# Performance work log

Measured on AMD Instinct MI355X. Metric: run time of the kernel, lower is better.

## Reference

```python
import jax, jax.numpy as jnp
import numpy as np

EMBED_DIM = 1024
NUM_HEADS = 16
HEAD_DIM = EMBED_DIM // NUM_HEADS


def setup_inputs() -> dict:
    key = jax.random.key(0)
    ks = jax.random.split(key, 6)
    std = 0.02
    x = jax.random.normal(ks[0], (2, 2048, EMBED_DIM), dtype=jnp.float32)
    Wq = jax.random.normal(ks[1], (EMBED_DIM, EMBED_DIM), dtype=jnp.float32) * std
    Wk = jax.random.normal(ks[2], (EMBED_DIM, EMBED_DIM), dtype=jnp.float32) * std
    Wv = jax.random.normal(ks[3], (EMBED_DIM, EMBED_DIM), dtype=jnp.float32) * std
    Wo = jax.random.normal(ks[4], (EMBED_DIM, EMBED_DIM), dtype=jnp.float32) * std
    Wf = jax.random.normal(ks[5], (NUM_HEADS, EMBED_DIM), dtype=jnp.float32) * std
    return {"x": x, "Wq": Wq, "Wk": Wk, "Wv": Wv, "Wo": Wo, "Wf": Wf}


def reference(x, Wq, Wk, Wv, Wo, Wf):
    b, n, d = x.shape
    h, hd = NUM_HEADS, HEAD_DIM
    # projections (nn.Linear without bias: y = x @ W^T)
    q = (x @ Wq.T).reshape(b, n, h, hd)
    k = (x @ Wk.T).reshape(b, n, h, hd)
    v = (x @ Wv.T).reshape(b, n, h, hd)
    # per-head log forget gate and its causal cumulative sum
    log_f = jax.nn.log_sigmoid(x @ Wf.T)          # [b, n, h]
    c = jnp.cumsum(log_f, axis=1)                 # [b, n, h], c_i = sum_{t<=i} log f_t
    cbh = c.transpose(0, 2, 1)                    # [b, h, n]
    scale = 1.0 / np.sqrt(hd).astype(np.float32)
    # scores s_ij = q_i.k_j * scale + (c_i - c_j)  (decay D_ij = sum_{t=j+1}^i log f_t)
    scores = jnp.einsum("bihd,bjhd->bhij", q, k) * scale
    scores = scores + cbh[:, :, :, None] - cbh[:, :, None, :]
    causal = jnp.tril(jnp.ones((n, n), dtype=bool))
    scores = jnp.where(causal, scores, -1e30)
    p = jax.nn.softmax(scores, axis=-1)           # [b, h, n, n]
    out = jnp.einsum("bhij,bjhd->bihd", p, v).reshape(b, n, d)
    return out @ Wo.T
```

## Files before the change

### kernel.cpp

```cpp
#include <hip/hip_runtime.h>

#define EMBED 1024
#define NHEAD 16
#define HD    64
#define SEQ   2048
#define BATCH 2
#define ROWS  (BATCH * SEQ)

typedef float f32x4 __attribute__((ext_vector_type(4)));
typedef short short8 __attribute__((ext_vector_type(8)));
typedef short short4v __attribute__((ext_vector_type(4)));
typedef unsigned short u16x4 __attribute__((ext_vector_type(4)));
typedef unsigned short u16x8 __attribute__((ext_vector_type(8)));
typedef unsigned u32x4 __attribute__((ext_vector_type(4)));
typedef unsigned u32x2 __attribute__((ext_vector_type(2)));

#define LOG2E 1.4426950408889634f

__device__ __forceinline__ unsigned short f2bf(float f) {
  unsigned int u = __builtin_bit_cast(unsigned int, f);
  u += 0x7fffu + ((u >> 16) & 1u);
  return (unsigned short)(u >> 16);
}

__device__ __forceinline__ unsigned cvtpk(float lo, float hi) {
  unsigned r;
  asm("v_cvt_pk_bf16_f32 %0, %1, %2" : "=v"(r) : "v"(lo), "v"(hi));
  return r;
}

#if __has_builtin(__builtin_amdgcn_exp2f)
#define EXP2(x) __builtin_amdgcn_exp2f(x)
#else
#define EXP2(x) exp2f(x)
#endif

__device__ __forceinline__ void gll16(const void* g, const void* l) {
  __builtin_amdgcn_global_load_lds(
      (const __attribute__((address_space(1))) unsigned int*)g,
      (__attribute__((address_space(3))) unsigned int*)l, 16, 0, 0);
}

__device__ __forceinline__ unsigned lds_addr(const void* p) {
  return (unsigned)(size_t)(__attribute__((address_space(3))) const void*)p;
}

__global__ __launch_bounds__(256) void cvt_all_kernel(
    const float* __restrict__ x,
    const float* __restrict__ w0, const float* __restrict__ w1,
    const float* __restrict__ w2, const float* __restrict__ w3,
    const float* __restrict__ wf,
    unsigned short* __restrict__ xo,
    unsigned short* __restrict__ o0, unsigned short* __restrict__ o1,
    unsigned short* __restrict__ o2, unsigned short* __restrict__ o3,
    unsigned short* __restrict__ wfh, unsigned short* __restrict__ wfl,
    unsigned* __restrict__ qkmaxu) {
  const int y = blockIdx.y;
  if (y < 4) {
    const float* in = (y == 0) ? w0 : (y == 1) ? w1 : (y == 2) ? w2 : w3;
    unsigned short* out = (y == 0) ? o0 : (y == 1) ? o1 : (y == 2) ? o2 : o3;
    const int i = blockIdx.x * 256 + threadIdx.x;
    const f32x4 v0 = reinterpret_cast<const f32x4*>(in)[2 * i];
    const f32x4 v1 = reinterpret_cast<const f32x4*>(in)[2 * i + 1];
    u16x8 o;
#pragma unroll
    for (int e = 0; e < 4; ++e) { o[e] = f2bf(v0[e]); o[e + 4] = f2bf(v1[e]); }
    reinterpret_cast<u16x8*>(out)[i] = o;
  } else if (y == 4) {
#pragma unroll
    for (int e = 0; e < 4; ++e) {
      const int i = e * 131072 + blockIdx.x * 256 + threadIdx.x;
      const f32x4 v0 = reinterpret_cast<const f32x4*>(x)[2 * i];
      const f32x4 v1 = reinterpret_cast<const f32x4*>(x)[2 * i + 1];
      u16x8 h;
#pragma unroll
      for (int q = 0; q < 4; ++q) { h[q] = f2bf(v0[q]); h[q + 4] = f2bf(v1[q]); }
      reinterpret_cast<u16x8*>(xo)[i] = h;
    }
  } else {
    if (blockIdx.x < 8) {
      const int i = blockIdx.x * 256 + threadIdx.x;
      const f32x4 v0 = reinterpret_cast<const f32x4*>(wf)[2 * i];
      const f32x4 v1 = reinterpret_cast<const f32x4*>(wf)[2 * i + 1];
      u16x8 h, l;
#pragma unroll
      for (int q = 0; q < 4; ++q) {
        h[q] = f2bf(v0[q]);
        l[q] = f2bf(v0[q] - __builtin_bit_cast(float, (unsigned)h[q] << 16));
        h[q + 4] = f2bf(v1[q]);
        l[q + 4] = f2bf(v1[q] - __builtin_bit_cast(float, (unsigned)h[q + 4] << 16));
      }
      reinterpret_cast<u16x8*>(wfh)[i] = h;
      reinterpret_cast<u16x8*>(wfl)[i] = l;
    } else if (blockIdx.x == 8) {
      if (threadIdx.x < 64) qkmaxu[threadIdx.x] = 0u;
    }
  }
}

__global__ __launch_bounds__(256) void gemm_wo_kernel(
    const unsigned short* __restrict__ A, const unsigned short* __restrict__ B,
    float* __restrict__ C) {
  __shared__ unsigned short Asm[64 * 64];
  __shared__ unsigned short Bsm[64 * 64];
  const int tid = threadIdx.x, wid = tid >> 6, lane = tid & 63;
  const int g = lane >> 4, l16 = lane & 15;
  const int wr = wid >> 1, wc = wid & 1;
  const int mb = blockIdx.y;
  const int nb = blockIdx.x;

  f32x4 acc[2][2] = {};

  for (int k0 = 0; k0 < EMBED; k0 += 64) {
    __syncthreads();
#pragma unroll
    for (int q = 0; q < 2; ++q) {
      const int base = (wid * 2 + q) * 1024;
      const int off = base + lane * 16;
      const int row = off >> 7;
      const int colel = (off & 127) >> 1;
      gll16(A + (size_t)(mb * 64 + row) * EMBED + k0 + colel, (const char*)Asm + base);
      gll16(B + (size_t)(nb * 64 + row) * EMBED + k0 + colel, (const char*)Bsm + base);
    }
    __syncthreads();

#pragma unroll
    for (int kc = 0; kc < 2; ++kc) {
      short8 am[2], bm[2];
#pragma unroll
      for (int mi = 0; mi < 2; ++mi)
        am[mi] = *reinterpret_cast<const short8*>(&Asm[(wr * 32 + mi * 16 + l16) * 64 + kc * 32 + g * 8]);
#pragma unroll
      for (int ni = 0; ni < 2; ++ni)
        bm[ni] = *reinterpret_cast<const short8*>(&Bsm[(wc * 32 + ni * 16 + l16) * 64 + kc * 32 + g * 8]);
#pragma unroll
      for (int mi = 0; mi < 2; ++mi)
#pragma unroll
        for (int ni = 0; ni < 2; ++ni)
          acc[mi][ni] = __builtin_amdgcn_mfma_f32_16x16x32_bf16(am[mi], bm[ni], acc[mi][ni], 0, 0, 0);
    }
  }

#pragma unroll
  for (int mi = 0; mi < 2; ++mi)
#pragma unroll
    for (int ni = 0; ni < 2; ++ni)
#pragma unroll
      for (int r = 0; r < 4; ++r) {
        const int m = mb * 64 + wr * 32 + mi * 16 + g * 4 + r;
        const int n = nb * 64 + wc * 32 + ni * 16 + l16;
        C[(size_t)m * EMBED + n] = acc[mi][ni][r];
      }
}

#define BAR() asm volatile("s_barrier" ::: "memory")
#define LGKM0()                                              \
  do {                                                       \
    asm volatile("s_waitcnt lgkmcnt(0)" ::: "memory");       \
    __builtin_amdgcn_sched_barrier(0);                       \
  } while (0)
#define VM(n_) asm volatile("s_waitcnt vmcnt(" #n_ ")" ::: "memory")

__global__ __launch_bounds__(512, 2) void gemm256_kernel(
    const unsigned short* __restrict__ A,
    const unsigned short* __restrict__ B0, const unsigned short* __restrict__ B1,
    const unsigned short* __restrict__ B2,
    unsigned short* __restrict__ C0, unsigned short* __restrict__ C1,
    unsigned short* __restrict__ C2, unsigned* __restrict__ qkmaxu,
    const float* __restrict__ x, const unsigned short* __restrict__ wfh,
    const unsigned short* __restrict__ wfl, float* __restrict__ carr) {
  __shared__ unsigned short sm[2][2][2][8192];
  const int tid = threadIdx.x, wid = tid >> 6, lane = tid & 63;
  const int g = lane >> 4, l16 = lane & 15;

  if (blockIdx.x >= 192) {
    const int bid2 = blockIdx.x - 192;
    const int tile = bid2 * 4 + (wid >> 1);
    const int half = wid & 1;
    const int row0 = tile * 16;
    const int k0 = half * 512;
    const float* xp = x + (size_t)(row0 + l16) * EMBED + k0 + g * 8;
    const unsigned short* whp = wfh + (size_t)l16 * EMBED + k0 + g * 8;
    const unsigned short* wlp = wfl + (size_t)l16 * EMBED + k0 + g * 8;
    f32x4 acc = {};
#pragma unroll
    for (int k = 0; k < 16; ++k) {
      const f32x4 v0 = *reinterpret_cast<const f32x4*>(xp + k * 32);
      const f32x4 v1 = *reinterpret_cast<const f32x4*>(xp + k * 32 + 4);
      short8 ah, al;
#pragma unroll
      for (int e = 0; e < 4; ++e) {
        const unsigned short h0 = f2bf(v0[e]);
        ah[e] = (short)h0;
        al[e] = (short)f2bf(v0[e] - __builtin_bit_cast(float, (unsigned)h0 << 16));
        const unsigned short h1 = f2bf(v1[e]);
        ah[e + 4] = (short)h1;
        al[e + 4] = (short)f2bf(v1[e] - __builtin_bit_cast(float, (unsigned)h1 << 16));
      }
      const short8 bh = *reinterpret_cast<const short8*>(whp + k * 32);
      const short8 bl = *reinterpret_cast<const short8*>(wlp + k * 32);
      acc = __builtin_amdgcn_mfma_f32_16x16x32_bf16(ah, bh, acc, 0, 0, 0);
      acc = __builtin_amdgcn_mfma_f32_16x16x32_bf16(ah, bl, acc, 0, 0, 0);
      acc = __builtin_amdgcn_mfma_f32_16x16x32_bf16(al, bh, acc, 0, 0, 0);
    }
    f32x4* red = reinterpret_cast<f32x4*>(sm);
    red[wid * 64 + lane] = acc;
    __syncthreads();
    if (half == 0) {
      const f32x4 a = red[wid * 64 + lane] + red[(wid + 1) * 64 + lane];
#pragma unroll
      for (int r = 0; r < 4; ++r) {
        const float s = a[r];
        const float ls = (fminf(s, 0.f) - log1pf(__expf(-fabsf(s)))) * LOG2E;
        const int n = row0 + g * 4 + r;
        const int b = n >> 11, nn = n & (SEQ - 1);
        carr[(size_t)(b * NHEAD + l16) * SEQ + nn] = ls;
      }
    }
    return;
  }

  const int wr = wid >> 2, wcol = wid & 3;
  const int mb = blockIdx.x / 12;
  const int nb = blockIdx.x % 12;
  const int which = nb >> 2;
  const int col0 = (nb & 3) * 256;
  const unsigned short* Bp = (which == 0) ? B0 : (which == 1) ? B1 : B2;
  unsigned short* Cp = (which == 0) ? C0 : (which == 1) ? C1 : C2;

  const int lane8 = lane & 7, laneHi = lane >> 3;
  const int colel = (lane8 ^ laneHi) * 8;
  int soff[2];
#pragma unroll
  for (int q = 0; q < 2; ++q)
    soff[q] = (q * 64 + wid * 8 + laneHi) * EMBED + colel;
  const unsigned short* Ag = A + (size_t)(mb * 256) * EMBED;
  const unsigned short* Bg = Bp + (size_t)col0 * EMBED;

  const int sw = (l16 & 7) << 4;
  const int cs0 = (0 | (g * 16)) ^ sw;
  const int cs1 = (64 | (g * 16)) ^ sw;
  const char* smB = (const char*)sm;
  const int aBase = wr * 16384 + l16 * 128;
  const int bBase = 32768 + (wcol >> 1) * 16384 + (wcol & 1) * 8192 + l16 * 128;

#define STG(buf_, ab_, half_, gsrc_, t_)                                               \
  do {                                                                                 \
    const unsigned short* gp_ = (gsrc_) + (size_t)(half_) * (128 * EMBED) + (t_) * 64; \
    char* lp_ = (char*)sm + (buf_) * 65536 + (ab_) * 32768 + (half_) * 16384 + wid * 1024; \
    gll16(gp_ + soff[0], lp_);                                                         \
    gll16(gp_ + soff[1], lp_ + 8192);                                                  \
  } while (0)

#define RD_A(buf_, row_, kc_) \
  (*reinterpret_cast<const short8*>(smB + (buf_) * 65536 + aBase + (row_) * 2048 + ((kc_) ? cs1 : cs0)))
#define RD_B(buf_, row_, kc_) \
  (*reinterpret_cast<const short8*>(smB + (buf_) * 65536 + bBase + (row_) * 2048 + ((kc_) ? cs1 : cs0)))

#define QUAD(mg_, ng_)                                                                   \
  do {                                                                                   \
    __builtin_amdgcn_s_setprio(1);                                                       \
    _Pragma("unroll") for (int kc_ = 0; kc_ < 2; ++kc_)                                  \
      _Pragma("unroll") for (int mi_ = 0; mi_ < 4; ++mi_)                                \
        _Pragma("unroll") for (int nj_ = 0; nj_ < 2; ++nj_)                              \
          acc[(mg_) * 4 + mi_][(ng_) * 2 + nj_] = __builtin_amdgcn_mfma_f32_16x16x32_bf16( \
              fa[mi_][kc_], fb[(ng_) * 2 + nj_][kc_], acc[(mg_) * 4 + mi_][(ng_) * 2 + nj_], 0, 0, 0); \
    __builtin_amdgcn_s_setprio(0);                                                       \
  } while (0)

#define KTILE4(BUF_, STG_P1, STG_P2, STG_P3, STG_P4_VM)                                  \
  do {                                                                                   \
    _Pragma("unroll") for (int mi_ = 0; mi_ < 4; ++mi_) {                                \
      fa[mi_][0] = RD_A(BUF_, mi_, 0);                                                   \
      fa[mi_][1] = RD_A(BUF_, mi_, 1);                                                   \
    }                                                                                    \
    _Pragma("unroll") for (int ni_ = 0; ni_ < 2; ++ni_) {                                \
      fb[ni_][0] = RD_B(BUF_, ni_, 0);                                                   \
      fb[ni_][1] = RD_B(BUF_, ni_, 1);                                                   \
    }                                                                                    \
    STG_P1;                                                                              \
    asm volatile("s_waitcnt lgkmcnt(8)" ::: "memory");                                   \
    BAR();                                                                               \
    LGKM0();                                                                             \
    QUAD(0, 0);                                                                          \
    BAR();                                                                               \
    _Pragma("unroll") for (int ni_ = 0; ni_ < 2; ++ni_) {                                \
      fb[2 + ni_][0] = RD_B(BUF_, 2 + ni_, 0);                                           \
      fb[2 + ni_][1] = RD_B(BUF_, 2 + ni_, 1);                                           \
    }                                                                                    \
    STG_P2;                                                                              \
    BAR();                                                                               \
    LGKM0();                                                                             \
    QUAD(0, 1);                                                                          \
    BAR();                                                                               \
    _Pragma("unroll") for (int mi_ = 0; mi_ < 4; ++mi_) {                                \
      fa[mi_][0] = RD_A(BUF_, 4 + mi_, 0);                                               \
      fa[mi_][1] = RD_A(BUF_, 4 + mi_, 1);                                               \
    }                                                                                    \
    STG_P3;                                                                              \
    BAR();                                                                               \
    LGKM0();                                                                             \
    QUAD(1, 0);                                                                          \
    BAR();                                                                               \
    STG_P4_VM;                                                                           \
    BAR();                                                                               \
    QUAD(1, 1);                                                                          \
    BAR();                                                                               \
  } while (0)

  short8 fa[4][2], fb[4][2];
  f32x4 acc[8][4] = {};

  STG(0, 0, 0, Ag, 0);
  STG(0, 1, 0, Bg, 0);
  STG(0, 0, 1, Ag, 0);
  STG(0, 1, 1, Bg, 0);
  STG(1, 1, 0, Bg, 1);
  STG(1, 1, 1, Bg, 1);
  VM(4);
  BAR();

  for (int it = 0; it < 8; ++it) {
    const int t1 = 2 * it + 1, t2 = 2 * it + 2, t3 = 2 * it + 3;
    const bool nl = (it < 7);
    KTILE4(0,
           STG(1, 0, 0, Ag, t1),
           STG(1, 0, 1, Ag, t1),
           if (nl) STG(0, 1, 0, Bg, t2),
           if (nl) { STG(0, 1, 1, Bg, t2); VM(4); } else VM(0));
    KTILE4(1,
           if (nl) STG(0, 0, 0, Ag, t2),
           if (nl) STG(0, 0, 1, Ag, t2),
           if (nl) STG(1, 1, 0, Bg, t3),
           if (nl) { STG(1, 1, 1, Bg, t3); VM(4); });
  }

  unsigned mxv = 0;
#pragma unroll
  for (int mi = 0; mi < 8; ++mi)
#pragma unroll
    for (int ni = 0; ni < 4; ++ni)
#pragma unroll
      for (int r = 0; r < 4; ++r) {
        const int m = mb * 256 + wr * 128 + mi * 16 + g * 4 + r;
        const int n = col0 + wcol * 64 + ni * 16 + l16;
        const unsigned short bv = f2bf(acc[mi][ni][r]);
        Cp[(size_t)m * EMBED + n] = bv;
        const unsigned a = bv & 0x7fffu;
        mxv = a > mxv ? a : mxv;
      }
  if (which < 2) {
#pragma unroll
    for (int mm = 1; mm < 64; mm <<= 1) {
      const unsigned o = __shfl_xor(mxv, mm);
      mxv = o > mxv ? o : mxv;
    }
    if (lane == 0) {
      const int bbat = (mb >= 8) ? 1 : 0;
      const int head = (nb & 3) * 4 + wcol;
      const int idx = which * 32 + bbat * 16 + head;
      atomicMax(&qkmaxu[idx], mxv << 16);
    }
  }
#undef STG
#undef RD_A
#undef RD_B
#undef QUAD
#undef KTILE4
}
#undef BAR
#undef LGKM0
#undef VM

__global__ void cumsum_kernel(float* __restrict__ c, const float* __restrict__ qkmax,
                              int* __restrict__ tstart) {
  __shared__ float tendS[32];
  __shared__ float cfirstS[32];
  const int bh = blockIdx.x;
  const int lane = threadIdx.x;
  float* p = c + (size_t)bh * SEQ;
  f32x4 vv[8];
  f32x4* vp = reinterpret_cast<f32x4*>(p + lane * 32);
#pragma unroll
  for (int q = 0; q < 8; ++q) vv[q] = vp[q];
  float run = 0.f;
#pragma unroll
  for (int q = 0; q < 8; ++q)
#pragma unroll
    for (int e = 0; e < 4; ++e) { run += vv[q][e]; vv[q][e] = run; }
  float s = run;
#pragma unroll
  for (int off = 1; off < 64; off <<= 1) {
    float u = __shfl_up(s, off);
    if (lane >= off) s += u;
  }
  const float excl = s - run;
#pragma unroll
  for (int q = 0; q < 8; ++q)
#pragma unroll
    for (int e = 0; e < 4; ++e) vv[q][e] += excl;
#pragma unroll
  for (int q = 0; q < 8; ++q) vp[q] = vv[q];

  if (lane & 1) tendS[lane >> 1] = s;
  else cfirstS[lane >> 1] = vv[0][0];
  __syncthreads();
  if (lane < 32) {
    const float qm = qkmax[bh];
    const float km = qkmax[32 + bh];
    const float thr = -41.f - 23.0832f * qm * km;
    const float c2imin = cfirstS[lane];
    int t = lane;
    while (t > 0 && (c2imin - tendS[t - 1] >= thr)) --t;
    tstart[bh * 32 + lane] = t;
  }
}

#define NINF (-3.0e38f)
#define SCL (0.125f * LOG2E)
#define BMARG 14.0f

#define TR_READ(dst, addr, OFF) \
  asm volatile("ds_read_b64_tr_b16 %0, %1 offset:" OFF : "=v"(dst) : "v"(addr))

__global__ __launch_bounds__(256) void fa_attn_kernel(
    const unsigned short* __restrict__ Q, const unsigned short* __restrict__ K,
    const unsigned short* __restrict__ V, const float* __restrict__ C,
    const int* __restrict__ tstartTab, unsigned short* __restrict__ O) {
  __shared__ unsigned short Ksm[2][4096];
  __shared__ unsigned short Vsm[2][4096];
  const int p = blockIdx.x;
  const int xcd = p & 7, s2 = p >> 3;
  const int hb = xcd * 4 + (s2 >> 5);
  const int qb = s2 & 31;
  const int hh = hb & 15, bb = hb >> 4;
  const int tid = threadIdx.x, wid = tid >> 6, lane = tid & 63;
  const int g = lane >> 4, l16 = lane & 15;
  const int i_base = qb * 64 + wid * 16;

  const float* cptr = C + (size_t)(bb * NHEAD + hh) * SEQ;

  int kOff[2], vOff[2];
#pragma unroll
  for (int qq = 0; qq < 2; ++qq) {
    const int q = wid * 2 + qq;
    {
      const int row = q * 8 + (lane >> 3);
      const int colel = ((lane & 7) ^ (lane >> 3)) * 8;
      kOff[qq] = row * EMBED + colel;
    }
    {
      const int dblk = q >> 1;
      const int j = (q & 1) * 32 + (lane >> 1);
      const int dlow = (lane & 1) * 8;
      vOff[qq] = j * EMBED + dblk * 16 + dlow;
    }
  }
  const unsigned short* Kbase = K + (size_t)bb * SEQ * EMBED + hh * HD;
  const unsigned short* Vbase = V + (size_t)bb * SEQ * EMBED + hh * HD;

  const int swz = (l16 & 7) << 4;
  const int koffB0 = ((0) | (g * 16)) ^ swz;
  const int koffB1 = ((64) | (g * 16)) ^ swz;
  const int krowB = l16 * 128;

#define STAGE(bufidx, tt)                                                              \
  do {                                                                                 \
    const unsigned short* kb_ = Kbase + (size_t)(tt) * 64 * EMBED;                     \
    const unsigned short* vb_ = Vbase + (size_t)(tt) * 64 * EMBED;                     \
    _Pragma("unroll") for (int qq = 0; qq < 2; ++qq) {                                 \
      gll16(kb_ + kOff[qq], (const char*)&Ksm[bufidx][0] + (wid * 2 + qq) * 1024);     \
      gll16(vb_ + vOff[qq], (const char*)&Vsm[bufidx][0] + (wid * 2 + qq) * 1024);     \
    }                                                                                  \
  } while (0)

  short8 qf0, qf1;
  {
    const unsigned short* qp = Q + (size_t)(bb * SEQ + i_base + l16) * EMBED + hh * HD + g * 8;
    qf0 = *reinterpret_cast<const short8*>(qp);
    qf1 = *reinterpret_cast<const short8*>(qp + 32);
  }
  const float c2i = cptr[i_base + l16];

  const int t_start = tstartTab[hb * 32 + qb];

  float mc_prev = (t_start == qb) ? c2i : cptr[t_start * 64 + 63];
  float l_ = 0.f;
  f32x4 accd[4] = {};

  STAGE(0, t_start);
  __syncthreads();

  int buf = 0;
  for (int t = t_start; t <= qb; ++t) {
    if (t < qb) STAGE(buf ^ 1, t + 1);
    const int kv0 = t * 64;
    const bool diag = (t == qb);
    const int nj = diag ? (wid + 1) : 4;

    const float mc_cur = diag ? c2i : cptr[kv0 + 63];
    const float corr = EXP2(mc_cur - mc_prev);
    mc_prev = mc_cur;
    const float mcB = mc_cur - BMARG;

    float pf[4][4];
    float lsum = 0.f;
#pragma unroll
    for (int jb = 0; jb < 4; ++jb) {
      if (jb < nj) {
        const char* kbp = (const char*)&Ksm[buf][0] + jb * 2048 + krowB;
        short8 kf0 = *reinterpret_cast<const short8*>(kbp + koffB0);
        short8 kf1 = *reinterpret_cast<const short8*>(kbp + koffB1);
        f32x4 s = {};
        __builtin_amdgcn_s_setprio(1);
        s = __builtin_amdgcn_mfma_f32_16x16x32_bf16(kf0, qf0, s, 0, 0, 0);
        s = __builtin_amdgcn_mfma_f32_16x16x32_bf16(kf1, qf1, s, 0, 0, 0);
        __builtin_amdgcn_s_setprio(0);
        const f32x4 cv = *reinterpret_cast<const f32x4*>(&cptr[kv0 + jb * 16 + g * 4]);
#pragma unroll
        for (int r = 0; r < 4; ++r) {
          float arg = __builtin_fmaf(s[r], SCL, mcB - cv[r]);
          if (diag && jb == wid && (g * 4 + r > l16)) arg = NINF;
          const float pv = EXP2(arg);
          pf[jb][r] = pv;
          lsum += pv;
        }
      } else {
#pragma unroll
        for (int r = 0; r < 4; ++r) pf[jb][r] = 0.f;
      }
    }
    l_ = l_ * corr + lsum;
#pragma unroll
    for (int d = 0; d < 4; ++d) accd[d] *= corr;

    u32x4 w0, w1;
    w0[0] = cvtpk(pf[0][0], pf[0][1]); w0[1] = cvtpk(pf[0][2], pf[0][3]);
    w0[2] = cvtpk(pf[1][0], pf[1][1]); w0[3] = cvtpk(pf[1][2], pf[1][3]);
    w1[0] = cvtpk(pf[2][0], pf[2][1]); w1[1] = cvtpk(pf[2][2], pf[2][3]);
    w1[2] = cvtpk(pf[3][0], pf[3][1]); w1[3] = cvtpk(pf[3][2], pf[3][3]);
    const short8 pb0 = __builtin_bit_cast(short8, w0);
    const short8 pb1 = __builtin_bit_cast(short8, w1);

    const unsigned vb0 = lds_addr(&Vsm[buf][0]) + lane * 8;
#pragma unroll
    for (int db = 0; db < 4; ++db) {
      const unsigned va = vb0 + db * 2048;
      short4v t0, t1, t2, t3;
      TR_READ(t0, va, "0");
      TR_READ(t1, va, "512");
      TR_READ(t2, va, "1024");
      TR_READ(t3, va, "1536");
      asm volatile("s_waitcnt lgkmcnt(0)" ::: "memory");
      __builtin_amdgcn_sched_barrier(0);
      short8 va0, va1;
#pragma unroll
      for (int e = 0; e < 4; ++e) {
        va0[e] = t0[e]; va0[e + 4] = t1[e];
        va1[e] = t2[e]; va1[e + 4] = t3[e];
      }
      __builtin_amdgcn_s_setprio(1);
      accd[db] = __builtin_amdgcn_mfma_f32_16x16x32_bf16(va0, pb0, accd[db], 0, 0, 0);
      accd[db] = __builtin_amdgcn_mfma_f32_16x16x32_bf16(va1, pb1, accd[db], 0, 0, 0);
      __builtin_amdgcn_s_setprio(0);
    }
    if (t < qb) __syncthreads();
    buf ^= 1;
  }

  l_ += __shfl_xor(l_, 16);
  l_ += __shfl_xor(l_, 32);
  const float inv = 1.0f / l_;
  unsigned short* op = O + (size_t)(bb * SEQ + i_base + l16) * EMBED + hh * HD;
#pragma unroll
  for (int db = 0; db < 4; ++db) {
    u32x2 o;
    o[0] = cvtpk(accd[db][0] * inv, accd[db][1] * inv);
    o[1] = cvtpk(accd[db][2] * inv, accd[db][3] * inv);
    *reinterpret_cast<u32x2*>(op + db * 16 + g * 4) = o;
  }
#undef STAGE
}

extern "C" void kernel_launch(void* const* d_in, const int* in_sizes, int n_in,
                              void* d_out, int out_size, void* d_ws, size_t ws_size,
                              hipStream_t stream) {
  const float* x = (const float*)d_in[0];
  const float* Wq = (const float*)d_in[1];
  const float* Wk = (const float*)d_in[2];
  const float* Wv = (const float*)d_in[3];
  const float* Wo = (const float*)d_in[4];
  const float* Wf = (const float*)d_in[5];
  float* out = (float*)d_out;

  char* ws = (char*)d_ws;
  const size_t SZ_X = (size_t)ROWS * EMBED * sizeof(unsigned short);
  const size_t SZ_W = (size_t)EMBED * EMBED * sizeof(unsigned short);
  const size_t SZ_WF = (size_t)NHEAD * EMBED * sizeof(unsigned short);
  unsigned short* xb = (unsigned short*)ws;   ws += SZ_X;
  unsigned short* Wqb = (unsigned short*)ws;  ws += SZ_W;
  unsigned short* Wkb = (unsigned short*)ws;  ws += SZ_W;
  unsigned short* Wvb = (unsigned short*)ws;  ws += SZ_W;
  unsigned short* Wob = (unsigned short*)ws;  ws += SZ_W;
  unsigned short* Wfh = (unsigned short*)ws;  ws += SZ_WF;
  unsigned short* Wfl = (unsigned short*)ws;  ws += SZ_WF;
  unsigned short* Qb = (unsigned short*)ws;   ws += SZ_X;
  unsigned short* Kb = (unsigned short*)ws;   ws += SZ_X;
  unsigned short* Vb = (unsigned short*)ws;   ws += SZ_X;
  unsigned short* attnb = (unsigned short*)ws; ws += SZ_X;
  float* carr = (float*)ws;                   ws += (size_t)BATCH * NHEAD * SEQ * sizeof(float);
  float* qkmax = (float*)ws;                  ws += 64 * sizeof(float);
  int* tstart = (int*)ws;                     ws += 1024 * sizeof(int);

  cvt_all_kernel<<<dim3(512, 6), 256, 0, stream>>>(
      x, Wq, Wk, Wv, Wo, Wf, xb, Wqb, Wkb, Wvb, Wob, Wfh, Wfl,
      (unsigned*)qkmax);

  gemm256_kernel<<<256, 512, 0, stream>>>(
      xb, Wqb, Wkb, Wvb, Qb, Kb, Vb, (unsigned*)qkmax, x, Wfh, Wfl, carr);

  cumsum_kernel<<<BATCH * NHEAD, 64, 0, stream>>>(carr, qkmax, tstart);

  fa_attn_kernel<<<1024, 256, 0, stream>>>(Qb, Kb, Vb, carr, tstart, attnb);

  gemm_wo_kernel<<<dim3(16, 64), 256, 0, stream>>>(attnb, Wob, out);
}
```

Before: 88.70 us.

## Replace pipelined 256x256 QKV GEMM with simpler 256x128 single-buffer tiles

The fused QKV projection GEMM drops its hand-scheduled double-buffered 256x256 tile pipeline in favour of a simple single-buffered 256x128 tile per block. Each loop iteration loads one K-slab, waits on vmcnt(0) and a barrier, then runs the MFMAs. This doubles the grid (384 GEMM blocks plus the forget-gate blocks) and raises the launch-bounds occupancy target, aiming for more parallelism across CUs. The cost is lost overlap between global loads and MFMA work, and lower data reuse per block.

After: 90.84 us. 2.4% more time.

```diff
diff --git a/kernel.cpp b/kernel.cpp
--- a/kernel.cpp
+++ b/kernel.cpp
@@ -153,15 +153,9 @@
       }
 }
 
-#define BAR() asm volatile("s_barrier" ::: "memory")
-#define LGKM0()                                              \
-  do {                                                       \
-    asm volatile("s_waitcnt lgkmcnt(0)" ::: "memory");       \
-    __builtin_amdgcn_sched_barrier(0);                       \
-  } while (0)
-#define VM(n_) asm volatile("s_waitcnt vmcnt(" #n_ ")" ::: "memory")
-
-__global__ __launch_bounds__(512, 2) void gemm256_kernel(
+#define VM0() asm volatile("s_waitcnt vmcnt(0)" ::: "memory")
+
+__global__ __launch_bounds__(512, 4) void gemm_qkv_kernel(
     const unsigned short* __restrict__ A,
     const unsigned short* __restrict__ B0, const unsigned short* __restrict__ B1,
     const unsigned short* __restrict__ B2,
@@ -169,12 +163,12 @@
     unsigned short* __restrict__ C2, unsigned* __restrict__ qkmaxu,
     const float* __restrict__ x, const unsigned short* __restrict__ wfh,
     const unsigned short* __restrict__ wfl, float* __restrict__ carr) {
-  __shared__ unsigned short sm[2][2][2][8192];
+  __shared__ unsigned short sm[24576];
   const int tid = threadIdx.x, wid = tid >> 6, lane = tid & 63;
   const int g = lane >> 4, l16 = lane & 15;
 
-  if (blockIdx.x >= 192) {
-    const int bid2 = blockIdx.x - 192;
+  if (blockIdx.x >= 384) {
+    const int bid2 = blockIdx.x - 384;
     const int tile = bid2 * 4 + (wid >> 1);
     const int half = wid & 1;
     const int row0 = tile * 16;
@@ -220,13 +214,15 @@
     return;
   }
 
-  const int wr = wid >> 2, wcol = wid & 3;
-  const int mb = blockIdx.x / 12;
-  const int nb = blockIdx.x % 12;
-  const int which = nb >> 2;
-  const int col0 = (nb & 3) * 256;
+  const int id = blockIdx.x;
+  const int mb = id / 24;
+  const int nb = id % 24;
+  const int which = nb >> 3;
+  const int coll = (nb & 7) * 128;
   const unsigned short* Bp = (which == 0) ? B0 : (which == 1) ? B1 : B2;
   unsigned short* Cp = (which == 0) ? C0 : (which == 1) ? C1 : C2;
+
+  const int wr = wid >> 1, wc = wid & 1;
 
   const int lane8 = lane & 7, laneHi = lane >> 3;
   const int colel = (lane8 ^ laneHi) * 8;
@@ -235,115 +231,61 @@
   for (int q = 0; q < 2; ++q)
     soff[q] = (q * 64 + wid * 8 + laneHi) * EMBED + colel;
   const unsigned short* Ag = A + (size_t)(mb * 256) * EMBED;
-  const unsigned short* Bg = Bp + (size_t)col0 * EMBED;
+  const unsigned short* Bg = Bp + (size_t)coll * EMBED;
 
   const int sw = (l16 & 7) << 4;
   const int cs0 = (0 | (g * 16)) ^ sw;
   const int cs1 = (64 | (g * 16)) ^ sw;
   const char* smB = (const char*)sm;
-  const int aBase = wr * 16384 + l16 * 128;
-  const int bBase = 32768 + (wcol >> 1) * 16384 + (wcol & 1) * 8192 + l16 * 128;
-
-#define STG(buf_, ab_, half_, gsrc_, t_)                                               \
-  do {                                                                                 \
-    const unsigned short* gp_ = (gsrc_) + (size_t)(half_) * (128 * EMBED) + (t_) * 64; \
-    char* lp_ = (char*)sm + (buf_) * 65536 + (ab_) * 32768 + (half_) * 16384 + wid * 1024; \
-    gll16(gp_ + soff[0], lp_);                                                         \
-    gll16(gp_ + soff[1], lp_ + 8192);                                                  \
+  const int aBase = (wr * 64 + l16) * 128;
+  const int bBase = 32768 + (wc * 64 + l16) * 128;
+
+#define STGU(uoff_, gsrc_)                                                 \
+  do {                                                                     \
+    char* lp_ = (char*)sm + (uoff_) + wid * 1024;                          \
+    gll16((gsrc_) + soff[0], lp_);                                         \
+    gll16((gsrc_) + soff[1], lp_ + 8192);                                  \
   } while (0)
 
-#define RD_A(buf_, row_, kc_) \
-  (*reinterpret_cast<const short8*>(smB + (buf_) * 65536 + aBase + (row_) * 2048 + ((kc_) ? cs1 : cs0)))
-#define RD_B(buf_, row_, kc_) \
-  (*reinterpret_cast<const short8*>(smB + (buf_) * 65536 + bBase + (row_) * 2048 + ((kc_) ? cs1 : cs0)))
-
-#define QUAD(mg_, ng_)                                                                   \
-  do {                                                                                   \
-    __builtin_amdgcn_s_setprio(1);                                                       \
-    _Pragma("unroll") for (int kc_ = 0; kc_ < 2; ++kc_)                                  \
-      _Pragma("unroll") for (int mi_ = 0; mi_ < 4; ++mi_)                                \
-        _Pragma("unroll") for (int nj_ = 0; nj_ < 2; ++nj_)                              \
-          acc[(mg_) * 4 + mi_][(ng_) * 2 + nj_] = __builtin_amdgcn_mfma_f32_16x16x32_bf16( \
-              fa[mi_][kc_], fb[(ng_) * 2 + nj_][kc_], acc[(mg_) * 4 + mi_][(ng_) * 2 + nj_], 0, 0, 0); \
-    __builtin_amdgcn_s_setprio(0);                                                       \
-  } while (0)
-
-#define KTILE4(BUF_, STG_P1, STG_P2, STG_P3, STG_P4_VM)                                  \
-  do {                                                                                   \
-    _Pragma("unroll") for (int mi_ = 0; mi_ < 4; ++mi_) {                                \
-      fa[mi_][0] = RD_A(BUF_, mi_, 0);                                                   \
-      fa[mi_][1] = RD_A(BUF_, mi_, 1);                                                   \
-    }                                                                                    \
-    _Pragma("unroll") for (int ni_ = 0; ni_ < 2; ++ni_) {                                \
-      fb[ni_][0] = RD_B(BUF_, ni_, 0);                                                   \
-      fb[ni_][1] = RD_B(BUF_, ni_, 1);                                                   \
-    }                                                                                    \
-    STG_P1;                                                                              \
-    asm volatile("s_waitcnt lgkmcnt(8)" ::: "memory");                                   \
-    BAR();                                                                               \
-    LGKM0();                                                                             \
-    QUAD(0, 0);                                                                          \
-    BAR();                                                                               \
-    _Pragma("unroll") for (int ni_ = 0; ni_ < 2; ++ni_) {                                \
-      fb[2 + ni_][0] = RD_B(BUF_, 2 + ni_, 0);                                           \
-      fb[2 + ni_][1] = RD_B(BUF_, 2 + ni_, 1);                                           \
-    }                                                                                    \
-    STG_P2;                                                                              \
-    BAR();                                                                               \
-    LGKM0();                                                                             \
-    QUAD(0, 1);                                                                          \
-    BAR();                                                                               \
-    _Pragma("unroll") for (int mi_ = 0; mi_ < 4; ++mi_) {                                \
-      fa[mi_][0] = RD_A(BUF_, 4 + mi_, 0);                                               \
-      fa[mi_][1] = RD_A(BUF_, 4 + mi_, 1);                                               \
-    }                                                                                    \
-    STG_P3;                                                                              \
-    BAR();                                                                               \
-    LGKM0();                                                                             \
-    QUAD(1, 0);                                                                          \
-    BAR();                                                                               \
-    STG_P4_VM;                                                                           \
-    BAR();                                                                               \
-    QUAD(1, 1);                                                                          \
-    BAR();                                                                               \
-  } while (0)
-
-  short8 fa[4][2], fb[4][2];
-  f32x4 acc[8][4] = {};
-
-  STG(0, 0, 0, Ag, 0);
-  STG(0, 1, 0, Bg, 0);
-  STG(0, 0, 1, Ag, 0);
-  STG(0, 1, 1, Bg, 0);
-  STG(1, 1, 0, Bg, 1);
-  STG(1, 1, 1, Bg, 1);
-  VM(4);
-  BAR();
-
-  for (int it = 0; it < 8; ++it) {
-    const int t1 = 2 * it + 1, t2 = 2 * it + 2, t3 = 2 * it + 3;
-    const bool nl = (it < 7);
-    KTILE4(0,
-           STG(1, 0, 0, Ag, t1),
-           STG(1, 0, 1, Ag, t1),
-           if (nl) STG(0, 1, 0, Bg, t2),
-           if (nl) { STG(0, 1, 1, Bg, t2); VM(4); } else VM(0));
-    KTILE4(1,
-           if (nl) STG(0, 0, 0, Ag, t2),
-           if (nl) STG(0, 0, 1, Ag, t2),
-           if (nl) STG(1, 1, 0, Bg, t3),
-           if (nl) { STG(1, 1, 1, Bg, t3); VM(4); });
+  f32x4 acc[4][4] = {};
+
+  for (int t = 0; t < 16; ++t) {
+    __syncthreads();
+    STGU(0, Ag + t * 64);
+    STGU(16384, Ag + (size_t)128 * EMBED + t * 64);
+    STGU(32768, Bg + t * 64);
+    VM0();
+    __syncthreads();
+
+#pragma unroll
+    for (int kc = 0; kc < 2; ++kc) {
+      const int cs = kc ? cs1 : cs0;
+      short8 am[4], bm[4];
+#pragma unroll
+      for (int mi = 0; mi < 4; ++mi)
+        am[mi] = *reinterpret_cast<const short8*>(smB + aBase + mi * 2048 + cs);
+#pragma unroll
+      for (int ni = 0; ni < 4; ++ni)
+        bm[ni] = *reinterpret_cast<const short8*>(smB + bBase + ni * 2048 + cs);
+      __builtin_amdgcn_s_setprio(1);
+#pragma unroll
+      for (int mi = 0; mi < 4; ++mi)
+#pragma unroll
+        for (int ni = 0; ni < 4; ++ni)
+          acc[mi][ni] = __builtin_amdgcn_mfma_f32_16x16x32_bf16(am[mi], bm[ni], acc[mi][ni], 0, 0, 0);
+      __builtin_amdgcn_s_setprio(0);
+    }
   }
 
   unsigned mxv = 0;
 #pragma unroll
-  for (int mi = 0; mi < 8; ++mi)
+  for (int mi = 0; mi < 4; ++mi)
 #pragma unroll
     for (int ni = 0; ni < 4; ++ni)
 #pragma unroll
       for (int r = 0; r < 4; ++r) {
-        const int m = mb * 256 + wr * 128 + mi * 16 + g * 4 + r;
-        const int n = col0 + wcol * 64 + ni * 16 + l16;
+        const int m = mb * 256 + wr * 64 + mi * 16 + g * 4 + r;
+        const int n = coll + wc * 64 + ni * 16 + l16;
         const unsigned short bv = f2bf(acc[mi][ni][r]);
         Cp[(size_t)m * EMBED + n] = bv;
         const unsigned a = bv & 0x7fffu;
@@ -357,20 +299,14 @@
     }
     if (lane == 0) {
       const int bbat = (mb >= 8) ? 1 : 0;
-      const int head = (nb & 3) * 4 + wcol;
+      const int head = (nb & 7) * 2 + wc;
       const int idx = which * 32 + bbat * 16 + head;
       atomicMax(&qkmaxu[idx], mxv << 16);
     }
   }
-#undef STG
-#undef RD_A
-#undef RD_B
-#undef QUAD
-#undef KTILE4
-}
-#undef BAR
-#undef LGKM0
-#undef VM
+#undef STGU
+}
+#undef VM0
 
 __global__ void cumsum_kernel(float* __restrict__ c, const float* __restrict__ qkmax,
                               int* __restrict__ tstart) {
@@ -616,7 +552,7 @@
       x, Wq, Wk, Wv, Wo, Wf, xb, Wqb, Wkb, Wvb, Wob, Wfh, Wfl,
       (unsigned*)qkmax);
 
-  gemm256_kernel<<<256, 512, 0, stream>>>(
+  gemm_qkv_kernel<<<448, 512, 0, stream>>>(
       xb, Wqb, Wkb, Wvb, Qb, Kb, Vb, (unsigned*)qkmax, x, Wfh, Wfl, carr);
 
   cumsum_kernel<<<BATCH * NHEAD, 64, 0, stream>>>(carr, qkmax, tstart);
```
